# Optimization experiments

Measured on AMD Instinct MI355X. Metric: run time of the kernel, lower is better.

Reference implementation:

```python
import jax, jax.numpy as jnp
import numpy as np
from jax import lax

B, LAT, NCLS, NGF, NC = 256, 100, 10, 128, 3
EPS = 1e-5


def _convt(x, w, stride, pad):
    # torch ConvTranspose2d(weight shape (Cin,Cout,k,k)) == lhs-dilated conv
    # with spatially flipped, in/out-swapped kernel and padding k-1-pad.
    k = w.shape[2]
    wt = jnp.flip(w, (2, 3)).transpose(1, 0, 2, 3)  # (Cout, Cin, k, k)
    p = k - 1 - pad
    return lax.conv_general_dilated(x, wt, (1, 1), [(p, p), (p, p)],
                                    lhs_dilation=(stride, stride),
                                    dimension_numbers=('NCHW', 'OIHW', 'NCHW'))


def _cconvt(xr, xi, wr, wi, br, bi, stride, pad):
    # complex transposed conv decomposed into 4 real convs (as torch does)
    yr = _convt(xr, wr, stride, pad) - _convt(xi, wi, stride, pad) + br[None, :, None, None]
    yi = _convt(xr, wi, stride, pad) + _convt(xi, wr, stride, pad) + bi[None, :, None, None]
    return yr, yi


def _cbn(xr, xi, grr, gri, gii, br, bi):
    # complex batchnorm: 2x2 covariance whitening over (N,H,W) + affine
    ax = (0, 2, 3)
    bc = lambda v: v[None, :, None, None]
    xr = xr - bc(xr.mean(ax))
    xi = xi - bc(xi.mean(ax))
    crr = (xr * xr).mean(ax) + EPS
    cii = (xi * xi).mean(ax) + EPS
    cri = (xr * xi).mean(ax)
    s = jnp.sqrt(crr * cii - cri * cri)          # sqrt(det)
    t = jnp.sqrt(crr + cii + 2.0 * s)            # sqrt(trace + 2 sqrt(det))
    inv = 1.0 / (s * t)
    rrr = (cii + s) * inv
    rii = (crr + s) * inv
    rri = -cri * inv
    yr = bc(rrr) * xr + bc(rri) * xi
    yi = bc(rri) * xr + bc(rii) * xi
    out_r = bc(grr) * yr + bc(gri) * yi + bc(br)
    out_i = bc(gri) * yr + bc(gii) * yi + bc(bi)
    return out_r, out_i


def _forward(noise_re, noise_im, labels, emb,
             w1r, w1i, b1r, b1i, g1rr, g1ri, g1ii, n1br, n1bi,
             w2r, w2i, b2r, b2i, g2rr, g2ri, g2ii, n2br, n2bi,
             w3r, w3i, b3r, b3i, g3rr, g3ri, g3ii, n3br, n3bi,
             w4r, w4i, b4r, b4i):
    lab = emb[labels][:, :, None, None]  # (B, NCLS, 1, 1); embedding is real
    xr = jnp.concatenate([noise_re, lab], axis=1)
    xi = jnp.concatenate([noise_im, jnp.zeros_like(lab)], axis=1)
    # 1x1 -> 4x4
    xr, xi = _cconvt(xr, xi, w1r, w1i, b1r, b1i, 1, 0)
    xr, xi = _cbn(xr, xi, g1rr, g1ri, g1ii, n1br, n1bi)
    xr, xi = jax.nn.relu(xr), jax.nn.relu(xi)  # CReLU
    # 4x4 -> 8x8
    xr, xi = _cconvt(xr, xi, w2r, w2i, b2r, b2i, 2, 1)
    xr, xi = _cbn(xr, xi, g2rr, g2ri, g2ii, n2br, n2bi)
    xr, xi = jax.nn.relu(xr), jax.nn.relu(xi)
    # 8x8 -> 16x16
    xr, xi = _cconvt(xr, xi, w3r, w3i, b3r, b3i, 2, 1)
    xr, xi = _cbn(xr, xi, g3rr, g3ri, g3ii, n3br, n3bi)
    xr, xi = jax.nn.relu(xr), jax.nn.relu(xi)
    # 16x16 -> 32x32
    xr, xi = _cconvt(xr, xi, w4r, w4i, b4r, b4i, 2, 1)
    return jnp.tanh(xr), jnp.tanh(xi)  # CTanh


def setup_inputs() -> dict:
    key = jax.random.key(0)
    ks = iter(jax.random.split(key, 40))
    rn = lambda shape, s: jax.random.normal(next(ks), shape, jnp.float32) * s
    d = {}
    d['noise_re'] = rn((B, LAT, 1, 1), 1.0)
    d['noise_im'] = rn((B, LAT, 1, 1), 1.0)
    d['labels'] = jax.random.randint(next(ks), (B,), 0, NCLS, jnp.int32)
    d['emb'] = rn((NCLS, NCLS), 1.0)
    chans = [(LAT + NCLS, NGF * 4), (NGF * 4, NGF * 2), (NGF * 2, NGF), (NGF, NC)]
    for i, (ci, co) in enumerate(chans, 1):
        d[f'w{i}r'] = rn((ci, co, 4, 4), 0.02)
        d[f'w{i}i'] = rn((ci, co, 4, 4), 0.02)
        d[f'b{i}r'] = jnp.zeros((co,), jnp.float32)
        d[f'b{i}i'] = jnp.zeros((co,), jnp.float32)
        if i < 4:
            d[f'g{i}rr'] = jnp.full((co,), 0.70710678, jnp.float32)
            d[f'g{i}ri'] = jnp.zeros((co,), jnp.float32)
            d[f'g{i}ii'] = jnp.full((co,), 0.70710678, jnp.float32)
            d[f'n{i}br'] = jnp.zeros((co,), jnp.float32)
            d[f'n{i}bi'] = jnp.zeros((co,), jnp.float32)
    return d


def reference(noise_re, noise_im, labels, emb,
              w1r, w1i, b1r, b1i, g1rr, g1ri, g1ii, n1br, n1bi,
              w2r, w2i, b2r, b2i, g2rr, g2ri, g2ii, n2br, n2bi,
              w3r, w3i, b3r, b3i, g3rr, g3ri, g3ii, n3br, n3bi,
              w4r, w4i, b4r, b4i):
    out_r, out_i = _forward(noise_re, noise_im, labels, emb,
                            w1r, w1i, b1r, b1i, g1rr, g1ri, g1ii, n1br, n1bi,
                            w2r, w2i, b2r, b2i, g2rr, g2ri, g2ii, n2br, n2bi,
                            w3r, w3i, b3r, b3i, g3rr, g3ri, g3ii, n3br, n3bi,
                            w4r, w4i, b4r, b4i)
    return out_r + 1j * out_i  # complex64 (B, NC, 32, 32)
```

## Files before the change

### kernel.cpp

```cpp
#include <hip/hip_runtime.h>
#include <hip/hip_bf16.h>
#include <math.h>

#define BATCH 256
#define LAT 100
#define NCLS 10
#define CIN0 110
#define C1 512
#define C2 256
#define C3 128
#define NCH 3
#define EPS 1e-5f
#define NCOPY 8

typedef __hip_bfloat16 bf16;
typedef short bf16x8 __attribute__((ext_vector_type(8)));
typedef float f32x4 __attribute__((ext_vector_type(4)));

__device__ __forceinline__ float b2f(bf16 v) { return __bfloat162float(v); }
__device__ __forceinline__ bf16 f2b(float v) { return __float2bfloat16(v); }
__device__ __forceinline__ float s2f(short s) {
    unsigned u = ((unsigned)(unsigned short)s) << 16;
    return __builtin_bit_cast(float, u);
}
__device__ __forceinline__ short f2s(float f) {
    bf16 b = __float2bfloat16(f);
    return *(short*)&b;
}

#define NB_W1 14336
#define NB_W2 32768
#define NB_W3 8192
#define NB_W4 256
#define NB_X0 224
#define NB_Z  36

__device__ __forceinline__ void w1prep_body(const float* wr, const float* wi, bf16* B, int idx) {
    if (idx >= 16384 * 224) return;
    int n = idx / 224, k = idx - n * 224;
    int p = n >> 10;
    int c = (n & 1023) >> 1;
    int part = n & 1;
    int pk = k >= 112; int ci = k - pk * 112;
    float v = 0.f;
    if (ci < CIN0) {
        size_t widx = ((size_t)ci * C1 + c) * 16 + p;
        float vr = wr[widx], vi = wi[widx];
        v = (part == 0) ? (pk ? -vi : vr) : (pk ? vr : vi);
    }
    B[idx] = f2b(v);
}

template<int CIN, int N>
__device__ __forceinline__ void wprep_panel_body(const float* wr, const float* wi, bf16* W,
                                                 size_t idx) {
    constexpr int TWOK = 8 * CIN, C2I = 2 * CIN;
    size_t per_cls = (size_t)2 * N * TWOK;
    if (idx >= 4 * per_cls) return;
    int cls = (int)(idx / per_cls);
    size_t r = idx - (size_t)cls * per_cls;
    size_t chunk_nb = (size_t)TWOK * 128;
    int nb = (int)(r / chunk_nb);
    int r2 = (int)(r - (size_t)nb * chunk_nb);
    int kb = r2 >> 12;
    int w = r2 & 4095;
    int f = w >> 9;
    int l = (w >> 3) & 63;
    int j = w & 7;
    int n_virt = nb * 128 + (f >> 2) * 64 + (f & 3) * 16 + (l & 15);
    int k = kb * 32 + (l >> 4) * 8 + j;
    int c = n_virt >> 1, part = n_virt & 1;
    int t = k / C2I;
    int q = k & (C2I - 1);
    int ci = q >> 1, p = q & 1;
    int py = cls >> 1, px = cls & 1;
    int a = t >> 1, e = t & 1;
    int kh = py ? (a ? 2 : 0) : (a ? 3 : 1);
    int kw = px ? (e ? 2 : 0) : (e ? 3 : 1);
    size_t widx = ((size_t)ci * N + c) * 16 + kh * 4 + kw;
    float vr = wr[widx], vi = wi[widx];
    float v = (part == 0) ? (p ? -vi : vr) : (p ? vr : vi);
    W[idx] = f2b(v);
}

__device__ __forceinline__ void wprep4_body(const float* wr, const float* wi, bf16* W, int idx) {
    if (idx >= 65536) return;
    int cls = idx >> 14, rem = idx & 16383;
    int py = cls >> 1, px = cls & 1;
    int n = rem >> 10, k = rem & 1023;
    float v = 0.f;
    if (n < NCH) {
        int t = k >> 8, q = k & 255;
        int ci = q >> 1, p = q & 1;
        int a = t >> 1, e = t & 1;
        int kh = py ? (a ? 2 : 0) : (a ? 3 : 1);
        int kw = px ? (e ? 2 : 0) : (e ? 3 : 1);
        size_t widx = ((size_t)ci * NCH + n) * 16 + kh * 4 + kw;
        v = p ? -wi[widx] : wr[widx];
    }
    W[idx] = f2b(v);
}

__device__ __forceinline__ void x0_body(const float* nre, const float* nim,
                                        const int* labels, const float* emb,
                                        bf16* A, int idx) {
    if (idx >= BATCH * 224) return;
    int b = idx / 224, k = idx - b * 224;
    int p = k >= 112; int ci = k - p * 112;
    float v = 0.f;
    if (ci < CIN0) {
        if (!p) v = (ci < LAT) ? nre[b * LAT + ci] : emb[labels[b] * NCLS + (ci - LAT)];
        else    v = (ci < LAT) ? nim[b * LAT + ci] : 0.f;
    }
    A[idx] = f2b(v);
}

__global__ void prep_combined(const float* __restrict__ w1r, const float* __restrict__ w1i,
                              const float* __restrict__ w2r, const float* __restrict__ w2i,
                              const float* __restrict__ w3r, const float* __restrict__ w3i,
                              const float* __restrict__ w4r, const float* __restrict__ w4i,
                              const float* __restrict__ nre, const float* __restrict__ nim,
                              const int* __restrict__ labels, const float* __restrict__ emb,
                              bf16* __restrict__ B1, bf16* __restrict__ W2all,
                              bf16* __restrict__ W3all, bf16* __restrict__ W4all,
                              bf16* __restrict__ x0bf, float* __restrict__ Szero) {
    int bid = blockIdx.x;
    if (bid < NB_W1) {
        w1prep_body(w1r, w1i, B1, bid * 256 + threadIdx.x);
    } else if (bid < NB_W1 + NB_W2) {
        wprep_panel_body<C1, C2>(w2r, w2i, W2all, (size_t)(bid - NB_W1) * 256 + threadIdx.x);
    } else if (bid < NB_W1 + NB_W2 + NB_W3) {
        wprep_panel_body<C2, C3>(w3r, w3i, W3all, (size_t)(bid - NB_W1 - NB_W2) * 256 + threadIdx.x);
    } else if (bid < NB_W1 + NB_W2 + NB_W3 + NB_W4) {
        wprep4_body(w4r, w4i, W4all, (bid - NB_W1 - NB_W2 - NB_W3) * 256 + threadIdx.x);
    } else if (bid < NB_W1 + NB_W2 + NB_W3 + NB_W4 + NB_X0) {
        x0_body(nre, nim, labels, emb, x0bf,
                (bid - NB_W1 - NB_W2 - NB_W3 - NB_W4) * 256 + threadIdx.x);
    } else {
        int idx = (bid - NB_W1 - NB_W2 - NB_W3 - NB_W4 - NB_X0) * 256 + threadIdx.x;
        if (idx < 35840) Szero[idx] = 0.f;
    }
}

__device__ __forceinline__ void epi_stats_flush(float* red, float* Scopy, int Cn,
                                                int cBaseGlobal, int tid, int lq,
                                                const int* clArr, float* s1,
                                                float* s2, float* sp, int isRe) {
    for (int i = tid; i < 320; i += 256) red[i] = 0.f;
    __syncthreads();
#pragma unroll
    for (int sn = 0; sn < 4; ++sn) {
        s1[sn] += __shfl_xor(s1[sn], 16, 64); s1[sn] += __shfl_xor(s1[sn], 32, 64);
        s2[sn] += __shfl_xor(s2[sn], 16, 64); s2[sn] += __shfl_xor(s2[sn], 32, 64);
        sp[sn] += __shfl_xor(sp[sn], 16, 64); sp[sn] += __shfl_xor(sp[sn], 32, 64);
    }
    if (lq == 0) {
#pragma unroll
        for (int sn = 0; sn < 4; ++sn) {
            int cl = clArr[sn];
            if (isRe) {
                atomicAdd(&red[cl * 5 + 0], s1[sn]);
                atomicAdd(&red[cl * 5 + 2], s2[sn]);
                atomicAdd(&red[cl * 5 + 4], sp[sn]);
            } else {
                atomicAdd(&red[cl * 5 + 1], s1[sn]);
                atomicAdd(&red[cl * 5 + 3], s2[sn]);
            }
        }
    }
    __syncthreads();
    for (int i = tid; i < 320; i += 256) {
        int cl = i / 5, st = i - cl * 5;
        atomicAdd(&Scopy[st * Cn + cBaseGlobal + cl], red[i]);
    }
}

__global__ __launch_bounds__(256, 1) void gemm1(
    const bf16* __restrict__ A, const bf16* __restrict__ B,
    const float* __restrict__ b1r, const float* __restrict__ b1i,
    bf16* __restrict__ Y, float* __restrict__ Sstat) {
    __shared__ short As[128][40];
    __shared__ short Bs[128][40];
    const int tid = threadIdx.x;
    const int mBase = blockIdx.x * 128, nBase = blockIdx.y * 128;
    const int wid = tid >> 6, lane = tid & 63;
    const int wm = (wid >> 1) * 64, wn = (wid & 1) * 64;
    const int lm = lane & 15, lq = lane >> 4;

    f32x4 acc[4][4] = {};

    for (int k0 = 0; k0 < 224; k0 += 32) {
#pragma unroll
        for (int it = 0; it < 2; ++it) {
            int slot = tid + it * 256;
            int row = slot >> 2, kc = (slot & 3) * 8;
            int k = k0 + kc;
            *(uint4*)(&As[row][kc]) = *(const uint4*)(A + (size_t)(mBase + row) * 224 + k);
            *(uint4*)(&Bs[row][kc]) = *(const uint4*)(B + (size_t)(nBase + row) * 224 + k);
        }
        __syncthreads();
        bf16x8 af[4], bfr[4];
#pragma unroll
        for (int s = 0; s < 4; ++s) {
            af[s]  = *(const bf16x8*)(&As[wm + s * 16 + lm][lq * 8]);
            bfr[s] = *(const bf16x8*)(&Bs[wn + s * 16 + lm][lq * 8]);
        }
#pragma unroll
        for (int sm = 0; sm < 4; ++sm)
#pragma unroll
            for (int sn = 0; sn < 4; ++sn)
                acc[sm][sn] = __builtin_amdgcn_mfma_f32_16x16x32_bf16(af[sm], bfr[sn], acc[sm][sn], 0, 0, 0);
        __syncthreads();
    }

    float s1[4] = {}, s2[4] = {}, sp[4] = {};
    int clArr[4];
#pragma unroll
    for (int sn = 0; sn < 4; ++sn) clArr[sn] = (wn + sn * 16 + lm) >> 1;
    const int part = lm & 1;

#pragma unroll
    for (int sm = 0; sm < 4; ++sm) {
#pragma unroll
        for (int v = 0; v < 4; ++v) {
            int m = mBase + wm + sm * 16 + lq * 4 + v;
#pragma unroll
            for (int sn = 0; sn < 4; ++sn) {
                int n = nBase + wn + sn * 16 + lm;
                int c = (n & 1023) >> 1;
                float bias = part ? b1i[c] : b1r[c];
                float val = acc[sm][sn][v] + bias;
                float pv = __shfl_xor(val, 1, 64);
                s1[sn] += val; s2[sn] += val * val;
                if (!part) sp[sn] += val * pv;
                Y[(size_t)m * 16384 + n] = f2b(val);
            }
        }
    }
    int copy = (blockIdx.y * gridDim.x + blockIdx.x) & (NCOPY - 1);
    epi_stats_flush((float*)As, Sstat + (size_t)copy * 5 * C1, C1,
                    (nBase & 1023) >> 1, tid, lq, clArr, s1, s2, sp, !part);
}

__global__ void bn_apply_v3(bf16* __restrict__ Y, const float* __restrict__ Scopies,
                            const float* __restrict__ grr, const float* __restrict__ gri,
                            const float* __restrict__ gii,
                            const float* __restrict__ betar, const float* __restrict__ betai,
                            int C, int total8, float invN) {
    __shared__ float coefs[6][512];
    for (int c = threadIdx.x; c < C; c += 256) {
        float sr = 0, si = 0, srr = 0, sii = 0, sri = 0;
        for (int cp = 0; cp < NCOPY; ++cp) {
            const float* S = Scopies + (size_t)cp * 5 * C;
            sr += S[c]; si += S[C + c]; srr += S[2 * C + c]; sii += S[3 * C + c]; sri += S[4 * C + c];
        }
        float mr = sr * invN, mi = si * invN;
        float crr = srr * invN - mr * mr + EPS;
        float cii = sii * invN - mi * mi + EPS;
        float cri = sri * invN - mr * mi;
        float s = sqrtf(crr * cii - cri * cri);
        float t = sqrtf(crr + cii + 2.f * s);
        float inv = 1.f / (s * t);
        float rrr = (cii + s) * inv, rii = (crr + s) * inv, rri = -cri * inv;
        float Grr = grr[c], Gri = gri[c], Gii = gii[c];
        float arr = Grr * rrr + Gri * rri, ari = Grr * rri + Gri * rii;
        float air = Gri * rrr + Gii * rri, aii = Gri * rri + Gii * rii;
        coefs[0][c] = arr; coefs[1][c] = ari;
        coefs[2][c] = betar[c] - arr * mr - ari * mi;
        coefs[3][c] = air; coefs[4][c] = aii;
        coefs[5][c] = betai[c] - air * mr - aii * mi;
    }
    __syncthreads();
    int idx = blockIdx.x * 256 + threadIdx.x;
    if (idx >= total8) return;
    size_t base = (size_t)idx * 8;
    int c0 = ((int)(base & (size_t)(2 * C - 1))) >> 1;
    bf16x8 v8 = *(const bf16x8*)(Y + base);
    bf16x8 o8;
#pragma unroll
    for (int u = 0; u < 4; ++u) {
        int c = c0 + u;
        float vr = s2f(v8[2 * u]), vi = s2f(v8[2 * u + 1]);
        o8[2 * u]     = f2s(fmaxf(coefs[0][c] * vr + coefs[1][c] * vi + coefs[2][c], 0.f));
        o8[2 * u + 1] = f2s(fmaxf(coefs[3][c] * vr + coefs[4][c] * vi + coefs[5][c], 0.f));
    }
    *(bf16x8*)(Y + base) = o8;
}

template<int CIN, int S, int N>
__global__ __launch_bounds__(256, 2) void gemm_convt_bd(
    const bf16* __restrict__ X, const bf16* __restrict__ Wall,
    const float* __restrict__ biasr, const float* __restrict__ biasi,
    bf16* __restrict__ Y, float* __restrict__ Sstat) {
    constexpr int TWOK = 8 * CIN, C2I = 2 * CIN, C2O = 2 * N, HOUT = 2 * S;
    constexpr int NSTEP = TWOK / 32;
    constexpr int CPS = C2I / 32;
    constexpr int LOG_CPS = (CIN == 512) ? 5 : 4;
    __shared__ short As[2][128][40];
    const int cls = blockIdx.z;
    const int py = cls >> 1, px = cls & 1;
    const int tid = threadIdx.x;
    const int mBase = blockIdx.x * 128, nBase = blockIdx.y * 128;
    const int wid = tid >> 6, lane = tid & 63;
    const int wm = (wid >> 1) * 64, wn = (wid & 1) * 64;
    const int lm = lane & 15, lq = lane >> 4;
    const int dh0 = py ? 1 : 0, dh1 = py ? 0 : -1;
    const int dw0 = px ? 1 : 0, dw1 = px ? 0 : -1;

    const bf16* Wp = Wall
        + ((size_t)(cls * (C2O / 128) + blockIdx.y) * (TWOK / 32)) * 4096
        + ((wn >> 6) * 4) * 512 + lane * 8;

    int rowA[2], kcA[2];
    long offT[2][4];
#pragma unroll
    for (int it = 0; it < 2; ++it) {
        int slot = tid + it * 256;
        rowA[it] = slot >> 2; kcA[it] = (slot & 3) * 8;
        int m = mBase + rowA[it];
        int b = m / (S * S); int rem = m - b * (S * S);
        int i = rem / S, j = rem % S;
#pragma unroll
        for (int t = 0; t < 4; ++t) {
            int a = t >> 1, e = t & 1;
            int ih = i + (a ? dh1 : dh0);
            int iw = j + (e ? dw1 : dw0);
            offT[it][t] = ((unsigned)ih < (unsigned)S && (unsigned)iw < (unsigned)S)
                ? (long)((b * S + ih) * S + iw) * C2I : -1L;
        }
    }

    auto loadA = [&](int kb, uint4* av) {
        int t = kb >> LOG_CPS;
        int q0 = (kb & (CPS - 1)) << 5;
#pragma unroll
        for (int it = 0; it < 2; ++it) {
            long o = offT[it][t];
            uint4 v = {0u, 0u, 0u, 0u};
            if (o >= 0)
                v = *(const uint4*)(X + o + q0 + kcA[it]);
            av[it] = v;
        }
    };

    f32x4 acc[4][4] = {};
    bf16x8 bq[4];
#pragma unroll
    for (int sn = 0; sn < 4; ++sn) bq[sn] = *(const bf16x8*)(Wp + sn * 512);

    {
        uint4 av[2];
        loadA(0, av);
#pragma unroll
        for (int it = 0; it < 2; ++it) *(uint4*)(&As[0][rowA[it]][kcA[it]]) = av[it];
    }
    __syncthreads();

    for (int ks = 0; ks < NSTEP; ++ks) {
        const int cur = ks & 1;
        uint4 av[2];
        if (ks + 1 < NSTEP) loadA(ks + 1, av);
        bf16x8 bcur[4];
#pragma unroll
        for (int sn = 0; sn < 4; ++sn) bcur[sn] = bq[sn];
        if (ks + 1 < NSTEP) {
            const bf16* Wn = Wp + (size_t)(ks + 1) * 4096;
#pragma unroll
            for (int sn = 0; sn < 4; ++sn) bq[sn] = *(const bf16x8*)(Wn + sn * 512);
        }
        bf16x8 af[4];
#pragma unroll
        for (int s = 0; s < 4; ++s)
            af[s] = *(const bf16x8*)(&As[cur][wm + s * 16 + lm][lq * 8]);
#pragma unroll
        for (int sm = 0; sm < 4; ++sm)
#pragma unroll
            for (int sn = 0; sn < 4; ++sn)
                acc[sm][sn] = __builtin_amdgcn_mfma_f32_16x16x32_bf16(af[sm], bcur[sn], acc[sm][sn], 0, 0, 0);
        if (ks + 1 < NSTEP) {
#pragma unroll
            for (int it = 0; it < 2; ++it) *(uint4*)(&As[1 - cur][rowA[it]][kcA[it]]) = av[it];
        }
        __syncthreads();
    }

    float s1[4] = {}, s2[4] = {}, sp[4] = {};
    int clArr[4];
#pragma unroll
    for (int sn = 0; sn < 4; ++sn) clArr[sn] = (wn + sn * 16 + lm) >> 1;
    const int part = lm & 1;

#pragma unroll
    for (int sm = 0; sm < 4; ++sm) {
#pragma unroll
        for (int v = 0; v < 4; ++v) {
            int m = mBase + wm + sm * 16 + lq * 4 + v;
            int b = m / (S * S); int rem = m - b * (S * S);
            int i = rem / S, j = rem % S;
            int oh = 2 * i + py, ow = 2 * j + px;
            size_t rowoff = (size_t)((b * HOUT + oh) * HOUT + ow) * C2O;
#pragma unroll
            for (int sn = 0; sn < 4; ++sn) {
                int n = nBase + wn + sn * 16 + lm;
                int c = n >> 1;
                float bias = part ? biasi[c] : biasr[c];
                float val = acc[sm][sn][v] + bias;
                float pv = __shfl_xor(val, 1, 64);
                s1[sn] += val; s2[sn] += val * val;
                if (!part) sp[sn] += val * pv;
                Y[rowoff + n] = f2b(val);
            }
        }
    }
    int copy = ((blockIdx.z * gridDim.y + blockIdx.y) * gridDim.x + blockIdx.x) & (NCOPY - 1);
    epi_stats_flush((float*)As, Sstat + (size_t)copy * 5 * N, N,
                    nBase >> 1, tid, lq, clArr, s1, s2, sp, !part);
}

__global__ __launch_bounds__(256, 2) void conv4_mfma(
    const bf16* __restrict__ X, const bf16* __restrict__ Wall,
    const float* __restrict__ br, float* __restrict__ out) {
    constexpr int S = 16, TWOK = 1024, C2I = 256;
    __shared__ short As[256][40];
    __shared__ short Bs[16][40];
    const int cls = blockIdx.z;
    const int py = cls >> 1, px = cls & 1;
    const bf16* W = Wall + (size_t)cls * 16 * TWOK;
    const int tid = threadIdx.x;
    const int mBase = blockIdx.x * 256;
    const int wid = tid >> 6, lane = tid & 63;
    const int wm = wid * 64;
    const int lm = lane & 15, lq = lane >> 4;
    const int dh0 = py ? 1 : 0, dh1 = py ? 0 : -1;
    const int dw0 = px ? 1 : 0, dw1 = px ? 0 : -1;

    int rowA[4], kcA[4];
    long offT[4][4];
#pragma unroll
    for (int it = 0; it < 4; ++it) {
        int slot = tid + it * 256;
        rowA[it] = slot >> 2; kcA[it] = (slot & 3) * 8;
        int m = mBase + rowA[it];
        int b = m >> 8; int rem = m & 255;
        int i = rem >> 4, j = rem & 15;
#pragma unroll
        for (int t = 0; t < 4; ++t) {
            int a = t >> 1, e = t & 1;
            int ih = i + (a ? dh1 : dh0);
            int iw = j + (e ? dw1 : dw0);
            offT[it][t] = ((unsigned)ih < (unsigned)S && (unsigned)iw < (unsigned)S)
                ? (long)((b * S + ih) * S + iw) * C2I : -1L;
        }
    }

    f32x4 acc[4] = {};

    for (int kb = 0; kb < TWOK / 32; ++kb) {
        int t = kb >> 3;
        int q0 = (kb & 7) << 5;
#pragma unroll
        for (int it = 0; it < 4; ++it) {
            long o = offT[it][t];
            uint4 v = {0u, 0u, 0u, 0u};
            if (o >= 0)
                v = *(const uint4*)(X + o + q0 + kcA[it]);
            *(uint4*)(&As[rowA[it]][kcA[it]]) = v;
        }
        if (tid < 64) {
            int row = tid >> 2, kc = (tid & 3) * 8;
            uint4 w = *(const uint4*)(W + (size_t)row * TWOK + kb * 32 + kc);
            *(uint4*)(&Bs[row][kc]) = w;
        }
        __syncthreads();
        bf16x8 bfr = *(const bf16x8*)(&Bs[lm][lq * 8]);
#pragma unroll
        for (int s = 0; s < 4; ++s) {
            bf16x8 af = *(const bf16x8*)(&As[wm + s * 16 + lm][lq * 8]);
            acc[s] = __builtin_amdgcn_mfma_f32_16x16x32_bf16(af, bfr, acc[s], 0, 0, 0);
        }
        __syncthreads();
    }

    int n = lm;
    if (n < NCH) {
        float bias = br[n];
#pragma unroll
        for (int s = 0; s < 4; ++s) {
#pragma unroll
            for (int v = 0; v < 4; ++v) {
                int m = mBase + wm + s * 16 + lq * 4 + v;
                int b = m >> 8; int rem = m & 255;
                int i = rem >> 4, j = rem & 15;
                int oh = 2 * i + py, ow = 2 * j + px;
                out[((size_t)(b * NCH + n) * 32 + oh) * 32 + ow] = tanhf(acc[s][v] + bias);
            }
        }
    }
}

extern "C" void kernel_launch(void* const* d_in, const int* in_sizes, int n_in,
                              void* d_out, int out_size, void* d_ws, size_t ws_size,
                              hipStream_t stream) {
    const float* noise_re = (const float*)d_in[0];
    const float* noise_im = (const float*)d_in[1];
    const int*   labels   = (const int*)d_in[2];
    const float* emb      = (const float*)d_in[3];
    const float* w1r = (const float*)d_in[4],  *w1i = (const float*)d_in[5];
    const float* b1r = (const float*)d_in[6],  *b1i = (const float*)d_in[7];
    const float* g1rr = (const float*)d_in[8], *g1ri = (const float*)d_in[9], *g1ii = (const float*)d_in[10];
    const float* n1br = (const float*)d_in[11], *n1bi = (const float*)d_in[12];
    const float* w2r = (const float*)d_in[13], *w2i = (const float*)d_in[14];
    const float* b2r = (const float*)d_in[15], *b2i = (const float*)d_in[16];
    const float* g2rr = (const float*)d_in[17], *g2ri = (const float*)d_in[18], *g2ii = (const float*)d_in[19];
    const float* n2br = (const float*)d_in[20], *n2bi = (const float*)d_in[21];
    const float* w3r = (const float*)d_in[22], *w3i = (const float*)d_in[23];
    const float* b3r = (const float*)d_in[24], *b3i = (const float*)d_in[25];
    const float* g3rr = (const float*)d_in[26], *g3ri = (const float*)d_in[27], *g3ii = (const float*)d_in[28];
    const float* n3br = (const float*)d_in[29], *n3bi = (const float*)d_in[30];
    const float* w4r = (const float*)d_in[31], *w4i = (const float*)d_in[32];
    const float* b4r = (const float*)d_in[33], *b4i = (const float*)d_in[34];

    char* ws = (char*)d_ws;
    bf16* y3cl = (bf16*)ws;
    bf16* x1cl = (bf16*)ws;
    bf16* B1    = (bf16*)(ws + 8388608);
    bf16* W2all = (bf16*)(ws + 15728640);
    bf16* y2cl  = (bf16*)(ws + 33554432);
    bf16* W3all = (bf16*)(ws + 50331648);
    bf16* x0bf  = (bf16*)(ws + 54547456);
    bf16* W4all = (bf16*)(ws + 54662144);
    float* S1 = (float*)(ws + 54793216);
    float* S2 = (float*)(ws + 54875136);
    float* S3 = (float*)(ws + 54916096);

    prep_combined<<<NB_W1 + NB_W2 + NB_W3 + NB_W4 + NB_X0 + NB_Z, 256, 0, stream>>>(
        w1r, w1i, w2r, w2i, w3r, w3i, w4r, w4i,
        noise_re, noise_im, labels, emb,
        B1, W2all, W3all, W4all, x0bf, S1);

    gemm1<<<dim3(2, 128), 256, 0, stream>>>(x0bf, B1, b1r, b1i, x1cl, S1);
    bn_apply_v3<<<2048, 256, 0, stream>>>(x1cl, S1, g1rr, g1ri, g1ii, n1br, n1bi,
                                          C1, 524288, 1.f / 4096.f);

    gemm_convt_bd<C1, 4, C2><<<dim3(32, 4, 4), 256, 0, stream>>>(x1cl, W2all, b2r, b2i, y2cl, S2);
    bn_apply_v3<<<4096, 256, 0, stream>>>(y2cl, S2, g2rr, g2ri, g2ii, n2br, n2bi,
                                          C2, 1048576, 1.f / 16384.f);

    gemm_convt_bd<C2, 8, C3><<<dim3(128, 2, 4), 256, 0, stream>>>(y2cl, W3all, b3r, b3i, y3cl, S3);
    bn_apply_v3<<<8192, 256, 0, stream>>>(y3cl, S3, g3rr, g3ri, g3ii, n3br, n3bi,
                                          C3, 2097152, 1.f / 65536.f);

    conv4_mfma<<<dim3(256, 1, 4), 256, 0, stream>>>(y3cl, W4all, b4r, (float*)d_out);
}
```

Baseline: 459.9 us.

## Remap workgroups XCD-aware, deepen register prefetch, raise occupancy hint

Workgroup IDs in both the transposed-conv GEMM and the final conv kernel are remapped so that consecutive logical tiles, which share A rows across output-channel tiles and parity classes, land on the same XCD chiplet's L2. The GEMM main loop now prefetches global A and B fragments two k-steps ahead instead of one, to hide more load latency. Launch bounds are raised from 2 to 3 waves per SIMD. The extra prefetch buffers add register pressure, which could cause spills under the tighter occupancy bound.

```diff
diff --git a/kernel.cpp b/kernel.cpp
--- a/kernel.cpp
+++ b/kernel.cpp
@@ -288,7 +288,7 @@
 }
 
 template<int CIN, int S, int N>
-__global__ __launch_bounds__(256, 2) void gemm_convt_bd(
+__global__ __launch_bounds__(256, 3) void gemm_convt_bd(
     const bf16* __restrict__ X, const bf16* __restrict__ Wall,
     const float* __restrict__ biasr, const float* __restrict__ biasi,
     bf16* __restrict__ Y, float* __restrict__ Sstat) {
@@ -296,11 +296,25 @@
     constexpr int NSTEP = TWOK / 32;
     constexpr int CPS = C2I / 32;
     constexpr int LOG_CPS = (CIN == 512) ? 5 : 4;
+    constexpr int GX = (BATCH * S * S) / 128;
+    constexpr int GY = C2O / 128;
+    constexpr int GZ = 4;
+    constexpr int NWG = GX * GY * GZ;
+    constexpr int CHUNK = NWG / 8;
+    constexpr int NYZ = GY * GZ;
     __shared__ short As[2][128][40];
-    const int cls = blockIdx.z;
+
+    const int phys = (blockIdx.z * GY + blockIdx.y) * GX + blockIdx.x;
+    const int L = (phys & 7) * CHUNK + (phys >> 3);
+    const int bx = L / NYZ;
+    const int ryz = L - bx * NYZ;
+    const int by = ryz % GY;
+    const int bz = ryz / GY;
+
+    const int cls = bz;
     const int py = cls >> 1, px = cls & 1;
     const int tid = threadIdx.x;
-    const int mBase = blockIdx.x * 128, nBase = blockIdx.y * 128;
+    const int mBase = bx * 128, nBase = by * 128;
     const int wid = tid >> 6, lane = tid & 63;
     const int wm = (wid >> 1) * 64, wn = (wid & 1) * 64;
     const int lm = lane & 15, lq = lane >> 4;
@@ -308,7 +322,7 @@
     const int dw0 = px ? 1 : 0, dw1 = px ? 0 : -1;
 
     const bf16* Wp = Wall
-        + ((size_t)(cls * (C2O / 128) + blockIdx.y) * (TWOK / 32)) * 4096
+        + ((size_t)(cls * (C2O / 128) + by) * (TWOK / 32)) * 4096
         + ((wn >> 6) * 4) * 512 + lane * 8;
 
     int rowA[2], kcA[2];
@@ -344,29 +358,34 @@
     };
 
     f32x4 acc[4][4] = {};
-    bf16x8 bq[4];
-#pragma unroll
-    for (int sn = 0; sn < 4; ++sn) bq[sn] = *(const bf16x8*)(Wp + sn * 512);
-
+
+    uint4 aNxt[2];
+    bf16x8 bCur[4], bNxt[4];
     {
-        uint4 av[2];
-        loadA(0, av);
-#pragma unroll
-        for (int it = 0; it < 2; ++it) *(uint4*)(&As[0][rowA[it]][kcA[it]]) = av[it];
+        uint4 a0[2];
+        loadA(0, a0);
+#pragma unroll
+        for (int sn = 0; sn < 4; ++sn) bCur[sn] = *(const bf16x8*)(Wp + sn * 512);
+        loadA(1, aNxt);
+        {
+            const bf16* Wn = Wp + 4096;
+#pragma unroll
+            for (int sn = 0; sn < 4; ++sn) bNxt[sn] = *(const bf16x8*)(Wn + sn * 512);
+        }
+#pragma unroll
+        for (int it = 0; it < 2; ++it) *(uint4*)(&As[0][rowA[it]][kcA[it]]) = a0[it];
     }
     __syncthreads();
 
     for (int ks = 0; ks < NSTEP; ++ks) {
         const int cur = ks & 1;
-        uint4 av[2];
-        if (ks + 1 < NSTEP) loadA(ks + 1, av);
-        bf16x8 bcur[4];
-#pragma unroll
-        for (int sn = 0; sn < 4; ++sn) bcur[sn] = bq[sn];
-        if (ks + 1 < NSTEP) {
-            const bf16* Wn = Wp + (size_t)(ks + 1) * 4096;
-#pragma unroll
-            for (int sn = 0; sn < 4; ++sn) bq[sn] = *(const bf16x8*)(Wn + sn * 512);
+        uint4 aFut[2];
+        bf16x8 bFut[4];
+        if (ks + 2 < NSTEP) {
+            loadA(ks + 2, aFut);
+            const bf16* Wn = Wp + (size_t)(ks + 2) * 4096;
+#pragma unroll
+            for (int sn = 0; sn < 4; ++sn) bFut[sn] = *(const bf16x8*)(Wn + sn * 512);
         }
         bf16x8 af[4];
 #pragma unroll
@@ -376,12 +395,16 @@
         for (int sm = 0; sm < 4; ++sm)
 #pragma unroll
             for (int sn = 0; sn < 4; ++sn)
-                acc[sm][sn] = __builtin_amdgcn_mfma_f32_16x16x32_bf16(af[sm], bcur[sn], acc[sm][sn], 0, 0, 0);
+                acc[sm][sn] = __builtin_amdgcn_mfma_f32_16x16x32_bf16(af[sm], bCur[sn], acc[sm][sn], 0, 0, 0);
         if (ks + 1 < NSTEP) {
 #pragma unroll
-            for (int it = 0; it < 2; ++it) *(uint4*)(&As[1 - cur][rowA[it]][kcA[it]]) = av[it];
+            for (int it = 0; it < 2; ++it) *(uint4*)(&As[1 - cur][rowA[it]][kcA[it]]) = aNxt[it];
         }
         __syncthreads();
+#pragma unroll
+        for (int it = 0; it < 2; ++it) aNxt[it] = aFut[it];
+#pragma unroll
+        for (int sn = 0; sn < 4; ++sn) { bCur[sn] = bNxt[sn]; bNxt[sn] = bFut[sn]; }
     }
 
     float s1[4] = {}, s2[4] = {}, sp[4] = {};
@@ -412,7 +435,7 @@
             }
         }
     }
-    int copy = ((blockIdx.z * gridDim.y + blockIdx.y) * gridDim.x + blockIdx.x) & (NCOPY - 1);
+    int copy = L & (NCOPY - 1);
     epi_stats_flush((float*)As, Sstat + (size_t)copy * 5 * N, N,
                     nBase >> 1, tid, lq, clArr, s1, s2, sp, !part);
 }
@@ -421,13 +444,19 @@
     const bf16* __restrict__ X, const bf16* __restrict__ Wall,
     const float* __restrict__ br, float* __restrict__ out) {
     constexpr int S = 16, TWOK = 1024, C2I = 256;
+    constexpr int GX = 256, GZ = 4, NWG = GX * GZ, CHUNK = NWG / 8;
     __shared__ short As[256][40];
     __shared__ short Bs[16][40];
-    const int cls = blockIdx.z;
+
+    const int phys = blockIdx.z * GX + blockIdx.x;
+    const int L = (phys & 7) * CHUNK + (phys >> 3);
+    const int bx = L >> 2;
+    const int cls = L & 3;
+
     const int py = cls >> 1, px = cls & 1;
     const bf16* W = Wall + (size_t)cls * 16 * TWOK;
     const int tid = threadIdx.x;
-    const int mBase = blockIdx.x * 256;
+    const int mBase = bx * 256;
     const int wid = tid >> 6, lane = tid & 63;
     const int wm = wid * 64;
     const int lm = lane & 15, lq = lane >> 4;
```

Measured after the change: 469.5 us. +2.1%, slower.
